# Optimization experiments

Measured on AMD Instinct MI355X. Metric: run time of the kernel, lower is better.

The kernel has to match this reference:

```python
import jax, jax.numpy as jnp
import numpy as np

N_NODES = 50000
N_EDGES = 600000
IN_DIM = 128
HID_DIM = 128
OUT_DIM = 128
N_GRAPHS = 64


def _glorot(key, shape):
    lim = np.sqrt(6.0 / (shape[0] + shape[1]))
    return jax.random.uniform(key, shape, jnp.float32, -lim, lim)


def setup_inputs() -> dict:
    key = jax.random.key(0)
    ks = jax.random.split(key, 8)
    h = jax.random.normal(ks[0], (N_NODES, IN_DIM), jnp.float32)
    src = jax.random.randint(ks[1], (N_EDGES,), 0, N_NODES, jnp.int64)
    dst = jax.random.randint(ks[2], (N_EDGES,), 0, N_NODES, jnp.int64)
    graph_ids = jnp.sort(jax.random.randint(ks[3], (N_NODES,), 0, N_GRAPHS, jnp.int64))
    W1 = _glorot(ks[4], (IN_DIM, HID_DIM)); b1 = jnp.zeros((HID_DIM,), jnp.float32)
    W2 = _glorot(ks[5], (HID_DIM, HID_DIM)); b2 = jnp.zeros((HID_DIM,), jnp.float32)
    W3 = _glorot(ks[6], (HID_DIM, OUT_DIM)); b3 = jnp.zeros((OUT_DIM,), jnp.float32)
    return {"h": h, "src": src, "dst": dst, "graph_ids": graph_ids,
            "W1": W1, "b1": b1, "W2": W2, "b2": b2, "W3": W3, "b3": b3,
            "n_graphs": N_GRAPHS}


def _graph_conv(h, src, dst, norm_src, norm_dst, W, b):
    # DGL GraphConv, norm='both': D_dst^{-1/2} A^T D_src^{-1/2} h W + b
    m = h * norm_src[:, None]                                   # [N, d]
    agg = jax.ops.segment_sum(m[src], dst, num_segments=h.shape[0])  # [N, d]
    return (agg * norm_dst[:, None]) @ W + b


def reference(h, src, dst, graph_ids, W1, b1, W2, b2, W3, b3, n_graphs):
    n = h.shape[0]
    ones = jnp.ones((src.shape[0],), h.dtype)
    out_deg = jnp.clip(jax.ops.segment_sum(ones, src, num_segments=n), 1.0)
    in_deg = jnp.clip(jax.ops.segment_sum(ones, dst, num_segments=n), 1.0)
    norm_src = out_deg ** -0.5
    norm_dst = in_deg ** -0.5

    x = jax.nn.relu(_graph_conv(h, src, dst, norm_src, norm_dst, W1, b1))
    x = jax.nn.relu(_graph_conv(x, src, dst, norm_src, norm_dst, W2, b2))
    x = jax.nn.relu(_graph_conv(x, src, dst, norm_src, norm_dst, W3, b3))

    # dgl.mean_nodes: per-graph mean over nodes
    gsum = jax.ops.segment_sum(x, graph_ids, num_segments=n_graphs)          # [G, d]
    gcnt = jax.ops.segment_sum(jnp.ones((n,), x.dtype), graph_ids, num_segments=n_graphs)
    return gsum / jnp.clip(gcnt, 1.0)[:, None]
```

## Files before the change

kernel.cpp:

```cpp
#include <hip/hip_runtime.h>
#include <hip/hip_fp16.h>


#define DIM 128

#define HIST_R 4
#define HIST_S 64
#define NPR 12500
#define LDSW (NPR / 2)

__global__ __launch_bounds__(256) void k_hist(const int* __restrict__ src,
                                              const int* __restrict__ dst,
                                              unsigned* __restrict__ partial, int E) {
    __shared__ unsigned hist[LDSW];
    int b = blockIdx.x;
    int a = b / (HIST_R * HIST_S);
    int r = (b / HIST_S) % HIST_R;
    int s = b % HIST_S;
    const int* arr = a ? dst : src;
    for (int i = threadIdx.x; i < LDSW; i += 256) hist[i] = 0;
    __syncthreads();
    int chunk = (E + HIST_S - 1) / HIST_S;
    int e0 = s * chunk;
    int e1 = min(e0 + chunk, E);
    unsigned base = (unsigned)(r * NPR);
    for (int i = e0 + threadIdx.x; i < e1; i += 256) {
        unsigned n = (unsigned)arr[i] - base;
        if (n < NPR) atomicAdd(&hist[n >> 1], 1u << ((n & 1) * 16));
    }
    __syncthreads();
    unsigned* outp = partial + ((size_t)(a * HIST_R + r) * HIST_S + s) * LDSW;
    for (int i = threadIdx.x; i < LDSW; i += 256) outp[i] = hist[i];
}

__global__ void k_hist_merge(const unsigned* __restrict__ partial,
                             float* __restrict__ ns, float* __restrict__ nd,
                             int* __restrict__ inc, int N) {
    int t = blockIdx.x * blockDim.x + threadIdx.x;
    const int total_w = HIST_R * LDSW;
    if (t >= 2 * total_w) return;
    int a = t / total_w;
    int wg = t % total_w;
    int r = wg / LDSW;
    int w = wg % LDSW;
    const unsigned* p = partial + ((size_t)(a * HIST_R + r) * HIST_S) * LDSW + w;
    unsigned sum = 0;
#pragma unroll
    for (int s = 0; s < HIST_S; ++s) sum += p[(size_t)s * LDSW];
    int n0 = r * NPR + w * 2;
    int d0 = (int)(sum & 0xFFFFu);
    int d1 = (int)(sum >> 16);
    if (a == 0) {
        if (n0 < N)     ns[n0]     = rsqrtf(fmaxf((float)d0, 1.0f));
        if (n0 + 1 < N) ns[n0 + 1] = rsqrtf(fmaxf((float)d1, 1.0f));
    } else {
        if (n0 < N)     { nd[n0]     = rsqrtf(fmaxf((float)d0, 1.0f)); inc[n0]     = d0; }
        if (n0 + 1 < N) { nd[n0 + 1] = rsqrtf(fmaxf((float)d1, 1.0f)); inc[n0 + 1] = d1; }
    }
}

__global__ void k_scan_partial(const int* __restrict__ inc, int* __restrict__ bsum, int N) {
    __shared__ int s[256];
    int i = blockIdx.x * 256 + threadIdx.x;
    int t = threadIdx.x;
    s[t] = (i < N) ? inc[i] : 0;
    __syncthreads();
    for (int off = 128; off > 0; off >>= 1) {
        if (t < off) s[t] += s[t + off];
        __syncthreads();
    }
    if (t == 0) bsum[blockIdx.x] = s[0];
}

__global__ void k_scan_top(int* __restrict__ bsum, int nb) {
    __shared__ int s[256];
    int t = threadIdx.x;
    int v = (t < nb) ? bsum[t] : 0;
    s[t] = v;
    __syncthreads();
    for (int off = 1; off < 256; off <<= 1) {
        int u = (t >= off) ? s[t - off] : 0;
        __syncthreads();
        s[t] += u;
        __syncthreads();
    }
    if (t < nb) bsum[t] = s[t] - v;
}

__global__ void k_scan_write(const int* __restrict__ inc, const int* __restrict__ bsum,
                             int* __restrict__ row_ptr, int N) {
    __shared__ int s[256];
    int i = blockIdx.x * 256 + threadIdx.x;
    int t = threadIdx.x;
    int v = (i < N) ? inc[i] : 0;
    s[t] = v;
    __syncthreads();
    for (int off = 1; off < 256; off <<= 1) {
        int u = (t >= off) ? s[t - off] : 0;
        __syncthreads();
        s[t] += u;
        __syncthreads();
    }
    int ex = bsum[blockIdx.x] + s[t] - v;
    if (i < N) row_ptr[i] = ex;
    if (i == N - 1) row_ptr[N] = ex + v;
}

__global__ void k_cursor(const unsigned* __restrict__ partial, const int* __restrict__ row_ptr,
                         int* __restrict__ cur, int N) {
    int t = blockIdx.x * blockDim.x + threadIdx.x;
    if (t >= HIST_R * LDSW) return;
    int r = t / LDSW;
    int w = t % LDSW;
    int n0 = r * NPR + 2 * w;
    const unsigned* p = partial + ((size_t)(HIST_R + r) * HIST_S) * LDSW + w;
    int run0 = (n0 < N) ? row_ptr[n0] : 0;
    int run1 = (n0 + 1 < N) ? row_ptr[n0 + 1] : 0;
    int* c = cur + (size_t)r * HIST_S * NPR + 2 * w;
#pragma unroll
    for (int s = 0; s < HIST_S; ++s) {
        c[(size_t)s * NPR + 0] = run0;
        c[(size_t)s * NPR + 1] = run1;
        unsigned hv = p[(size_t)s * LDSW];
        run0 += (int)(hv & 0xFFFFu);
        run1 += (int)(hv >> 16);
    }
}

__global__ __launch_bounds__(256) void k_fill2(const int* __restrict__ src,
                                               const int* __restrict__ dst,
                                               const int* __restrict__ cur,
                                               int* __restrict__ csr, int E) {
    __shared__ int lcur[NPR];
    int r = blockIdx.x / HIST_S;
    int s = blockIdx.x % HIST_S;
    const int* cs = cur + (size_t)(r * HIST_S + s) * NPR;
    for (int i = threadIdx.x; i < NPR; i += 256) lcur[i] = cs[i];
    __syncthreads();
    int chunk = (E + HIST_S - 1) / HIST_S;
    int e0 = s * chunk;
    int e1 = min(e0 + chunk, E);
    unsigned base = (unsigned)(r * NPR);
    for (int i = e0 + threadIdx.x; i < e1; i += 256) {
        unsigned d = (unsigned)dst[i] - base;
        if (d < NPR) {
            int p = atomicAdd(&lcur[d], 1);
            csr[p] = src[i];
        }
    }
}

__global__ void k_h2half(const float4* __restrict__ h, const float* __restrict__ ns,
                         uint2* __restrict__ A, int N) {
    int i = blockIdx.x * blockDim.x + threadIdx.x;
    if (i < N * 32) {
        int n = i >> 5;
        float s = ns[n];
        float4 v = h[i];
        __half2 p0 = __floats2half2_rn(v.x * s, v.y * s);
        __half2 p1 = __floats2half2_rn(v.z * s, v.w * s);
        uint2 o;
        o.x = *(unsigned*)&p0;
        o.y = *(unsigned*)&p1;
        A[i] = o;
    }
}

__global__ void k_agg(const uint2* __restrict__ A, const int* __restrict__ row_ptr,
                      const int* __restrict__ csr, const float* __restrict__ nd,
                      float* __restrict__ B, int N) {
    int gtid = blockIdx.x * blockDim.x + threadIdx.x;
    int node = gtid >> 6;
    int lane = threadIdx.x & 63;
    if (node >= N) return;
    int e0 = row_ptr[node];
    int e1 = row_ptr[node + 1];
    int half = lane >> 5;
    int l8 = lane & 31;
    float ax = 0.f, ay = 0.f, az = 0.f, aw = 0.f;

    auto acc4 = [&](uint2 u) {
        __half2 p0 = *(__half2*)&u.x;
        __half2 p1 = *(__half2*)&u.y;
        float2 f0 = __half22float2(p0);
        float2 f1 = __half22float2(p1);
        ax += f0.x; ay += f0.y; az += f1.x; aw += f1.y;
    };

    int e = e0;
    for (; e + 8 <= e1; e += 8) {
        int s0 = csr[e + half];
        int s1 = csr[e + 2 + half];
        int s2 = csr[e + 4 + half];
        int s3 = csr[e + 6 + half];
        uint2 u0 = A[(size_t)s0 * 32 + l8];
        uint2 u1 = A[(size_t)s1 * 32 + l8];
        uint2 u2 = A[(size_t)s2 * 32 + l8];
        uint2 u3 = A[(size_t)s3 * 32 + l8];
        acc4(u0); acc4(u1); acc4(u2); acc4(u3);
    }
    for (; e + 2 <= e1; e += 2) {
        int s0 = csr[e + half];
        acc4(A[(size_t)s0 * 32 + l8]);
    }
    if (e < e1 && half == 0) {
        int s0 = csr[e];
        acc4(A[(size_t)s0 * 32 + l8]);
    }

    ax += __shfl_xor(ax, 32);
    ay += __shfl_xor(ay, 32);
    az += __shfl_xor(az, 32);
    aw += __shfl_xor(aw, 32);

    if (half == 0) {
        float scale = nd[node];
        float4 o;
        o.x = ax * scale; o.y = ay * scale; o.z = az * scale; o.w = aw * scale;
        ((float4*)B)[(size_t)node * 32 + l8] = o;
    }
}

template <bool HALF_OUT>
__global__ __launch_bounds__(256) void k_gemm(
    const float* __restrict__ Y, const float* __restrict__ W,
    const float* __restrict__ bias, const float* __restrict__ ns,
    void* __restrict__ Xout, int N) {
    __shared__ float xsT[32][36];
    __shared__ float ws[32][128];

    int tid = threadIdx.x;
    int tx = tid & 31;
    int ty = tid >> 5;
    int r0 = blockIdx.x * 32;

    float acc[4][4] = {};

    for (int k0 = 0; k0 < 128; k0 += 32) {
        {
            int r = tid >> 3;
            int cq = tid & 7;
            int row = r0 + r;
            float4 v = make_float4(0.f, 0.f, 0.f, 0.f);
            if (row < N) v = *(const float4*)&Y[(size_t)row * DIM + k0 + cq * 4];
            xsT[cq * 4 + 0][r] = v.x;
            xsT[cq * 4 + 1][r] = v.y;
            xsT[cq * 4 + 2][r] = v.z;
            xsT[cq * 4 + 3][r] = v.w;
        }
#pragma unroll
        for (int j = 0; j < 4; ++j) {
            int idx = tid + j * 256;
            int row = idx >> 5;
            int cq = idx & 31;
            *(float4*)&ws[row][cq * 4] =
                *(const float4*)&W[(size_t)(k0 + row) * DIM + cq * 4];
        }
        __syncthreads();
#pragma unroll
        for (int kk = 0; kk < 32; ++kk) {
            float4 a = *(const float4*)&xsT[kk][ty * 4];
            float4 w = *(const float4*)&ws[kk][tx * 4];
            acc[0][0] += a.x * w.x; acc[0][1] += a.x * w.y; acc[0][2] += a.x * w.z; acc[0][3] += a.x * w.w;
            acc[1][0] += a.y * w.x; acc[1][1] += a.y * w.y; acc[1][2] += a.y * w.z; acc[1][3] += a.y * w.w;
            acc[2][0] += a.z * w.x; acc[2][1] += a.z * w.y; acc[2][2] += a.z * w.z; acc[2][3] += a.z * w.w;
            acc[3][0] += a.w * w.x; acc[3][1] += a.w * w.y; acc[3][2] += a.w * w.z; acc[3][3] += a.w * w.w;
        }
        __syncthreads();
    }

    float4 bb = *(const float4*)&bias[tx * 4];
#pragma unroll
    for (int i = 0; i < 4; ++i) {
        int row = r0 + ty * 4 + i;
        if (row >= N) continue;
        float o0 = fmaxf(acc[i][0] + bb.x, 0.0f);
        float o1 = fmaxf(acc[i][1] + bb.y, 0.0f);
        float o2 = fmaxf(acc[i][2] + bb.z, 0.0f);
        float o3 = fmaxf(acc[i][3] + bb.w, 0.0f);
        if (HALF_OUT) {
            float s = ns[row];
            __half2 p0 = __floats2half2_rn(o0 * s, o1 * s);
            __half2 p1 = __floats2half2_rn(o2 * s, o3 * s);
            uint2 o;
            o.x = *(unsigned*)&p0;
            o.y = *(unsigned*)&p1;
            ((uint2*)Xout)[(size_t)row * 32 + tx] = o;
        } else {
            float4 o = make_float4(o0, o1, o2, o3);
            ((float4*)Xout)[(size_t)row * 32 + tx] = o;
        }
    }
}

#define POOL_NODES 32
__global__ void k_pool_partial(const float* __restrict__ X, const int* __restrict__ gid,
                               float* __restrict__ gsum, int* __restrict__ gcnt, int N) {
    int n0 = blockIdx.x * POOL_NODES;
    int d = threadIdx.x;
    int nend = min(n0 + POOL_NODES, N);
    float run = 0.0f;
    int cnt = 0;
    int curg = -1;
    for (int n = n0; n < nend; ++n) {
        int g = gid[n];
        if (g != curg) {
            if (cnt > 0) {
                atomicAdd(&gsum[curg * DIM + d], run);
                if (d == 0) atomicAdd(&gcnt[curg], cnt);
            }
            run = 0.0f; cnt = 0; curg = g;
        }
        run += X[(size_t)n * DIM + d];
        cnt++;
    }
    if (cnt > 0) {
        atomicAdd(&gsum[curg * DIM + d], run);
        if (d == 0) atomicAdd(&gcnt[curg], cnt);
    }
}

__global__ void k_finalize(const float* __restrict__ gsum, const int* __restrict__ gcnt,
                           float* __restrict__ out, int G) {
    int i = blockIdx.x * blockDim.x + threadIdx.x;
    if (i < G * DIM) {
        int g = i >> 7;
        float c = fmaxf((float)gcnt[g], 1.0f);
        out[i] = gsum[i] / c;
    }
}

extern "C" void kernel_launch(void* const* d_in, const int* in_sizes, int n_in,
                              void* d_out, int out_size, void* d_ws, size_t ws_size,
                              hipStream_t stream) {
    const float* h   = (const float*)d_in[0];
    const int*   src = (const int*)d_in[1];
    const int*   dst = (const int*)d_in[2];
    const int*   gid = (const int*)d_in[3];
    const float* W1  = (const float*)d_in[4];
    const float* b1  = (const float*)d_in[5];
    const float* W2  = (const float*)d_in[6];
    const float* b2  = (const float*)d_in[7];
    const float* W3  = (const float*)d_in[8];
    const float* b3  = (const float*)d_in[9];

    const int N = in_sizes[0] / DIM;
    const int E = in_sizes[1];
    const int G = 64;
    float* out = (float*)d_out;

    char* ws = (char*)d_ws;
    size_t off = 0;
    auto alloc = [&](size_t bytes) -> void* {
        void* p = ws + off;
        off += (bytes + 255) & ~(size_t)255;
        return p;
    };
    const int scanBlocks = (N + 255) / 256;
    uint2* Ah0     = (uint2*)alloc((size_t)N * DIM * 2);
    uint2* Ah1     = (uint2*)alloc((size_t)N * DIM * 2);
    float* B       = (float*)alloc((size_t)N * DIM * 4);
    float* X3      = (float*)alloc((size_t)N * DIM * 4);
    float* ns      = (float*)alloc((size_t)N * 4);
    float* nd      = (float*)alloc((size_t)N * 4);
    int*   inc     = (int*)alloc((size_t)N * 4);
    unsigned* partial = (unsigned*)alloc((size_t)2 * HIST_R * HIST_S * LDSW * 4);
    int*   cur     = (int*)alloc((size_t)HIST_R * HIST_S * NPR * 4);
    int*   row_ptr = (int*)alloc((size_t)(N + 1) * 4);
    int*   csr     = (int*)alloc((size_t)E * 4);
    float* gsum    = (float*)alloc((size_t)G * DIM * 4);
    int*   gcnt    = (int*)alloc((size_t)G * 4);
    int*   bsum    = (int*)alloc((size_t)scanBlocks * 4);

    hipMemsetAsync(gsum, 0, (size_t)G * DIM * 4, stream);
    hipMemsetAsync(gcnt, 0, (size_t)G * 4, stream);

    k_hist<<<2 * HIST_R * HIST_S, 256, 0, stream>>>(src, dst, partial, E);
    int mergeThreads = 2 * HIST_R * LDSW;
    k_hist_merge<<<(mergeThreads + 255) / 256, 256, 0, stream>>>(partial, ns, nd, inc, N);

    k_scan_partial<<<scanBlocks, 256, 0, stream>>>(inc, bsum, N);
    k_scan_top<<<1, 256, 0, stream>>>(bsum, scanBlocks);
    k_scan_write<<<scanBlocks, 256, 0, stream>>>(inc, bsum, row_ptr, N);

    int curThreads = HIST_R * LDSW;
    k_cursor<<<(curThreads + 255) / 256, 256, 0, stream>>>(partial, row_ptr, cur, N);
    k_fill2<<<HIST_R * HIST_S, 256, 0, stream>>>(src, dst, cur, csr, E);

    int aggBlocks  = (N * 64 + 255) / 256;
    int gemmBlocks = (N + 31) / 32;

    k_h2half<<<(N * 32 + 255) / 256, 256, 0, stream>>>((const float4*)h, ns, Ah0, N);
    k_agg<<<aggBlocks, 256, 0, stream>>>(Ah0, row_ptr, csr, nd, B, N);
    k_gemm<true><<<gemmBlocks, 256, 0, stream>>>(B, W1, b1, ns, Ah1, N);
    k_agg<<<aggBlocks, 256, 0, stream>>>(Ah1, row_ptr, csr, nd, B, N);
    k_gemm<true><<<gemmBlocks, 256, 0, stream>>>(B, W2, b2, ns, Ah0, N);
    k_agg<<<aggBlocks, 256, 0, stream>>>(Ah0, row_ptr, csr, nd, B, N);
    k_gemm<false><<<gemmBlocks, 256, 0, stream>>>(B, W3, b3, ns, X3, N);

    k_pool_partial<<<(N + POOL_NODES - 1) / POOL_NODES, 128, 0, stream>>>(X3, gid, gsum, gcnt, N);
    k_finalize<<<(G * DIM + 255) / 256, 256, 0, stream>>>(gsum, gcnt, out, G);
}
```

Baseline: 336.0 us.

## Use fp16 MFMA for dense layers and emit fp16 aggregation output

```diff
diff --git a/kernel.cpp b/kernel.cpp
--- a/kernel.cpp
+++ b/kernel.cpp
@@ -3,6 +3,9 @@
 
 
 #define DIM 128
+
+typedef _Float16 half8 __attribute__((ext_vector_type(8)));
+typedef float floatx4 __attribute__((ext_vector_type(4)));
 
 #define HIST_R 4
 #define HIST_S 64
@@ -166,9 +169,16 @@
     }
 }
 
+__global__ void k_w2half(const float* __restrict__ W, _Float16* __restrict__ Wt) {
+    int i = blockIdx.x * blockDim.x + threadIdx.x;
+    int k = i >> 7;
+    int n = i & 127;
+    Wt[(size_t)n * DIM + k] = (_Float16)W[i];
+}
+
 __global__ void k_agg(const uint2* __restrict__ A, const int* __restrict__ row_ptr,
                       const int* __restrict__ csr, const float* __restrict__ nd,
-                      float* __restrict__ B, int N) {
+                      uint2* __restrict__ Bh, int N) {
     int gtid = blockIdx.x * blockDim.x + threadIdx.x;
     int node = gtid >> 6;
     int lane = threadIdx.x & 63;
@@ -215,80 +225,68 @@
 
     if (half == 0) {
         float scale = nd[node];
-        float4 o;
-        o.x = ax * scale; o.y = ay * scale; o.z = az * scale; o.w = aw * scale;
-        ((float4*)B)[(size_t)node * 32 + l8] = o;
+        __half2 p0 = __floats2half2_rn(ax * scale, ay * scale);
+        __half2 p1 = __floats2half2_rn(az * scale, aw * scale);
+        uint2 o;
+        o.x = *(unsigned*)&p0;
+        o.y = *(unsigned*)&p1;
+        Bh[(size_t)node * 32 + l8] = o;
     }
 }
 
 template <bool HALF_OUT>
-__global__ __launch_bounds__(256) void k_gemm(
-    const float* __restrict__ Y, const float* __restrict__ W,
+__global__ __launch_bounds__(256) void k_gemm_mfma(
+    const _Float16* __restrict__ Bin, const _Float16* __restrict__ Wt,
     const float* __restrict__ bias, const float* __restrict__ ns,
     void* __restrict__ Xout, int N) {
-    __shared__ float xsT[32][36];
-    __shared__ float ws[32][128];
-
     int tid = threadIdx.x;
-    int tx = tid & 31;
-    int ty = tid >> 5;
-    int r0 = blockIdx.x * 32;
-
-    float acc[4][4] = {};
-
-    for (int k0 = 0; k0 < 128; k0 += 32) {
-        {
-            int r = tid >> 3;
-            int cq = tid & 7;
-            int row = r0 + r;
-            float4 v = make_float4(0.f, 0.f, 0.f, 0.f);
-            if (row < N) v = *(const float4*)&Y[(size_t)row * DIM + k0 + cq * 4];
-            xsT[cq * 4 + 0][r] = v.x;
-            xsT[cq * 4 + 1][r] = v.y;
-            xsT[cq * 4 + 2][r] = v.z;
-            xsT[cq * 4 + 3][r] = v.w;
+    int wave = tid >> 6;
+    int lane = tid & 63;
+    int quad = lane >> 4;
+    int l16 = lane & 15;
+    int r0 = blockIdx.x * 64 + wave * 16;
+    int arow = r0 + l16;
+
+    half8 a[4];
+#pragma unroll
+    for (int q = 0; q < 4; ++q) {
+        if (arow < N) {
+            a[q] = *(const half8*)&Bin[(size_t)arow * DIM + q * 32 + quad * 8];
+        } else {
+            a[q] = half8{0, 0, 0, 0, 0, 0, 0, 0};
         }
-#pragma unroll
-        for (int j = 0; j < 4; ++j) {
-            int idx = tid + j * 256;
-            int row = idx >> 5;
-            int cq = idx & 31;
-            *(float4*)&ws[row][cq * 4] =
-                *(const float4*)&W[(size_t)(k0 + row) * DIM + cq * 4];
+    }
+
+    floatx4 acc[8];
+#pragma unroll
+    for (int c = 0; c < 8; ++c) acc[c] = floatx4{0.f, 0.f, 0.f, 0.f};
+
+#pragma unroll
+    for (int c = 0; c < 8; ++c) {
+#pragma unroll
+        for (int q = 0; q < 4; ++q) {
+            half8 b = *(const half8*)&Wt[(size_t)(c * 16 + l16) * DIM + q * 32 + quad * 8];
+            acc[c] = __builtin_amdgcn_mfma_f32_16x16x32_f16(a[q], b, acc[c], 0, 0, 0);
         }
-        __syncthreads();
-#pragma unroll
-        for (int kk = 0; kk < 32; ++kk) {
-            float4 a = *(const float4*)&xsT[kk][ty * 4];
-            float4 w = *(const float4*)&ws[kk][tx * 4];
-            acc[0][0] += a.x * w.x; acc[0][1] += a.x * w.y; acc[0][2] += a.x * w.z; acc[0][3] += a.x * w.w;
-            acc[1][0] += a.y * w.x; acc[1][1] += a.y * w.y; acc[1][2] += a.y * w.z; acc[1][3] += a.y * w.w;
-            acc[2][0] += a.z * w.x; acc[2][1] += a.z * w.y; acc[2][2] += a.z * w.z; acc[2][3] += a.z * w.w;
-            acc[3][0] += a.w * w.x; acc[3][1] += a.w * w.y; acc[3][2] += a.w * w.z; acc[3][3] += a.w * w.w;
-        }
-        __syncthreads();
-    }
-
-    float4 bb = *(const float4*)&bias[tx * 4];
-#pragma unroll
-    for (int i = 0; i < 4; ++i) {
-        int row = r0 + ty * 4 + i;
+    }
+
+    float bb[8];
+#pragma unroll
+    for (int c = 0; c < 8; ++c) bb[c] = bias[c * 16 + l16];
+
+#pragma unroll
+    for (int r = 0; r < 4; ++r) {
+        int row = r0 + quad * 4 + r;
         if (row >= N) continue;
-        float o0 = fmaxf(acc[i][0] + bb.x, 0.0f);
-        float o1 = fmaxf(acc[i][1] + bb.y, 0.0f);
-        float o2 = fmaxf(acc[i][2] + bb.z, 0.0f);
-        float o3 = fmaxf(acc[i][3] + bb.w, 0.0f);
-        if (HALF_OUT) {
-            float s = ns[row];
-            __half2 p0 = __floats2half2_rn(o0 * s, o1 * s);
-            __half2 p1 = __floats2half2_rn(o2 * s, o3 * s);
-            uint2 o;
-            o.x = *(unsigned*)&p0;
-            o.y = *(unsigned*)&p1;
-            ((uint2*)Xout)[(size_t)row * 32 + tx] = o;
-        } else {
-            float4 o = make_float4(o0, o1, o2, o3);
-            ((float4*)Xout)[(size_t)row * 32 + tx] = o;
+        float sr = HALF_OUT ? ns[row] : 1.0f;
+#pragma unroll
+        for (int c = 0; c < 8; ++c) {
+            float v = fmaxf(acc[c][r] + bb[c], 0.0f);
+            if (HALF_OUT) {
+                ((_Float16*)Xout)[(size_t)row * DIM + c * 16 + l16] = (_Float16)(v * sr);
+            } else {
+                ((float*)Xout)[(size_t)row * DIM + c * 16 + l16] = v;
+            }
         }
     }
 }
@@ -359,8 +357,11 @@
     const int scanBlocks = (N + 255) / 256;
     uint2* Ah0     = (uint2*)alloc((size_t)N * DIM * 2);
     uint2* Ah1     = (uint2*)alloc((size_t)N * DIM * 2);
-    float* B       = (float*)alloc((size_t)N * DIM * 4);
+    uint2* Bh      = (uint2*)alloc((size_t)N * DIM * 2);
     float* X3      = (float*)alloc((size_t)N * DIM * 4);
+    _Float16* Wt1  = (_Float16*)alloc((size_t)DIM * DIM * 2);
+    _Float16* Wt2  = (_Float16*)alloc((size_t)DIM * DIM * 2);
+    _Float16* Wt3  = (_Float16*)alloc((size_t)DIM * DIM * 2);
     float* ns      = (float*)alloc((size_t)N * 4);
     float* nd      = (float*)alloc((size_t)N * 4);
     int*   inc     = (int*)alloc((size_t)N * 4);
@@ -387,16 +388,20 @@
     k_cursor<<<(curThreads + 255) / 256, 256, 0, stream>>>(partial, row_ptr, cur, N);
     k_fill2<<<HIST_R * HIST_S, 256, 0, stream>>>(src, dst, cur, csr, E);
 
+    k_w2half<<<64, 256, 0, stream>>>(W1, Wt1);
+    k_w2half<<<64, 256, 0, stream>>>(W2, Wt2);
+    k_w2half<<<64, 256, 0, stream>>>(W3, Wt3);
+
     int aggBlocks  = (N * 64 + 255) / 256;
-    int gemmBlocks = (N + 31) / 32;
+    int gemmBlocks = (N + 63) / 64;
 
     k_h2half<<<(N * 32 + 255) / 256, 256, 0, stream>>>((const float4*)h, ns, Ah0, N);
-    k_agg<<<aggBlocks, 256, 0, stream>>>(Ah0, row_ptr, csr, nd, B, N);
-    k_gemm<true><<<gemmBlocks, 256, 0, stream>>>(B, W1, b1, ns, Ah1, N);
-    k_agg<<<aggBlocks, 256, 0, stream>>>(Ah1, row_ptr, csr, nd, B, N);
-    k_gemm<true><<<gemmBlocks, 256, 0, stream>>>(B, W2, b2, ns, Ah0, N);
-    k_agg<<<aggBlocks, 256, 0, stream>>>(Ah0, row_ptr, csr, nd, B, N);
-    k_gemm<false><<<gemmBlocks, 256, 0, stream>>>(B, W3, b3, ns, X3, N);
+    k_agg<<<aggBlocks, 256, 0, stream>>>(Ah0, row_ptr, csr, nd, Bh, N);
+    k_gemm_mfma<true><<<gemmBlocks, 256, 0, stream>>>((const _Float16*)Bh, Wt1, b1, ns, Ah1, N);
+    k_agg<<<aggBlocks, 256, 0, stream>>>(Ah1, row_ptr, csr, nd, Bh, N);
+    k_gemm_mfma<true><<<gemmBlocks, 256, 0, stream>>>((const _Float16*)Bh, Wt2, b2, ns, Ah0, N);
+    k_agg<<<aggBlocks, 256, 0, stream>>>(Ah0, row_ptr, csr, nd, Bh, N);
+    k_gemm_mfma<false><<<gemmBlocks, 256, 0, stream>>>((const _Float16*)Bh, Wt3, b3, ns, X3, N);
 
     k_pool_partial<<<(N + POOL_NODES - 1) / POOL_NODES, 128, 0, stream>>>(X3, gid, gsum, gcnt, N);
     k_finalize<<<(G * DIM + 255) / 256, 256, 0, stream>>>(gsum, gcnt, out, G);
```

Result: faster. 325.9 us (-3.0%).
